# Performance work log

Hardware: AMD Instinct MI355X
Metric: run time of the kernel (lower is better)

Reference implementation:

```python
import jax, jax.numpy as jnp
import numpy as np

LATENT_DIM = 32
NB_LABEL = 10
B = 4096


def _conv4(x, w, b):
    # stride-4 kernel-4 conv == non-overlapping 4x4 patch contraction
    Bn, C, H, W = x.shape
    xp = x.reshape(Bn, C, H // 4, 4, W // 4, 4)
    return jnp.einsum('bcipjq,ocpq->boij', xp, w) + b[None, :, None, None]


def _deconv4(x, w, b):
    # stride-4 kernel-4 ConvTranspose2d, padding 0: each pixel expands to a 4x4 block
    Bn, C, H, W = x.shape
    y = jnp.einsum('bcij,copq->boipjq', x, w)  # w: (Cin, Cout, 4, 4)
    return y.reshape(Bn, w.shape[1], H * 4, W * 4) + b[None, :, None, None]


def setup_inputs() -> dict:
    key = jax.random.key(0)
    ks = jax.random.split(key, 24)
    s = 0.05

    def rn(k, shape, scale=s):
        return jax.random.normal(k, shape, dtype=jnp.float32) * scale

    return {
        'x': jax.random.normal(ks[0], (B, 1, 64, 64), dtype=jnp.float32),
        'z': jax.random.normal(ks[1], (B, NB_LABEL), dtype=jnp.float32),
        'u_in': jax.random.normal(ks[2], (B, 2), dtype=jnp.float32),
        'conv1_w': rn(ks[3], (16, 1, 4, 4)), 'conv1_b': rn(ks[4], (16,)),
        'conv2_w': rn(ks[5], (64, 16, 4, 4)), 'conv2_b': rn(ks[6], (64,)),
        'conv3_w': rn(ks[7], (256, 64, 4, 4)), 'conv3_b': rn(ks[8], (256,)),
        'w_xz': rn(ks[9], (32, 256)),
        'w_label': rn(ks[10], (NB_LABEL, 32)),
        'w_zd1': rn(ks[11], (LATENT_DIM, NB_LABEL)),
        'w_zd2': rn(ks[12], (LATENT_DIM, NB_LABEL)),
        'w_xu': rn(ks[13], (32, 256)),
        'w_mu': rn(ks[14], (2, 32)),
        'w_logvar': rn(ks[15], (2, 32)),
        'tc_w': rn(ks[16], (LATENT_DIM, 256, 2)),
        'tc_b': rn(ks[17], (LATENT_DIM, 256)),
        'dec3_w': rn(ks[18], (256, 64, 4, 4)), 'dec3_b': rn(ks[19], (64,)),
        'dec2_w': rn(ks[20], (64, 16, 4, 4)), 'dec2_b': rn(ks[21], (16,)),
        'dec1_w': rn(ks[22], (16, 1, 4, 4)), 'dec1_b': jnp.zeros((1,), dtype=jnp.float32),
    }


def reference(x, z, u_in, conv1_w, conv1_b, conv2_w, conv2_b, conv3_w, conv3_b,
              w_xz, w_label, w_zd1, w_zd2, w_xu, w_mu, w_logvar, tc_w, tc_b,
              dec3_w, dec3_b, dec2_w, dec2_b, dec1_w, dec1_b):
    h = jax.nn.relu(_conv4(x, conv1_w, conv1_b))
    h = jax.nn.relu(_conv4(h, conv2_w, conv2_b))
    h = jax.nn.relu(_conv4(h, conv3_w, conv3_b))
    h = h.reshape(h.shape[0], -1)                       # (B, 256)

    x_z = jax.nn.relu(h @ w_xz.T)                       # (B, 32)
    z_logit = x_z @ w_label.T                           # (B, 10)

    key = jax.random.key(42)
    k_cat, k_eps = jax.random.split(key)
    z_hat = jax.random.categorical(k_cat, z_logit, axis=-1)       # (B,)
    z_onehot = jax.nn.one_hot(z_hat, NB_LABEL, dtype=z_logit.dtype)
    z_d1 = z_onehot @ w_zd1.T                           # (B, 32)
    z_d2 = z_onehot @ w_zd2.T                           # (B, 32)

    x_u = jax.nn.relu(h @ w_xu.T)                       # (B, 32)
    mu = x_u @ w_mu.T                                   # (B, 2)
    logvar = x_u @ w_logvar.T                           # (B, 2)
    std = jnp.exp(0.5 * logvar)
    eps = jax.random.normal(k_eps, std.shape, dtype=std.dtype)
    u_out = eps * std + mu                              # (B, 2)

    # all 32 tiny Linear(2->256)+ReLU collapsed into one batched einsum
    trans = u_out[:, None, :] + jnp.stack([z_d1, z_d2], axis=-1)   # (B, 32, 2)
    x_hat = jax.nn.relu(jnp.einsum('bic,ioc->bio', trans, tc_w) + tc_b[None]).sum(axis=1)  # (B, 256)
    transfo_d1 = trans[:, :, 0]                         # (B, 32)
    transfo_d2 = trans[:, :, 1]

    d = x_hat.reshape(-1, 256, 1, 1)
    d = jax.nn.relu(_deconv4(d, dec3_w, dec3_b))        # (B, 64, 4, 4)
    d = jax.nn.relu(_deconv4(d, dec2_w, dec2_b))        # (B, 16, 16, 16)
    x_hat_logit = _deconv4(d, dec1_w, dec1_b)           # (B, 1, 64, 64)

    return (z_logit, z_hat.reshape(-1, 1), mu, logvar, u_out, x_hat_logit, transfo_d1, transfo_d2)
```

## Files before the change

### kernel.cpp

```cpp
#include <hip/hip_runtime.h>
#include <stdint.h>

#define B_TOT 4096

#define OFF_ZL 0
#define OFF_ZH 40960
#define OFF_MU 45056
#define OFF_LV 53248
#define OFF_UO 61440
#define OFF_XL 69632
#define OFF_T1 16846848
#define OFF_T2 16977920

typedef __attribute__((ext_vector_type(8))) short bf16x8;
typedef __attribute__((ext_vector_type(4))) float f32x4;

__device__ __forceinline__ unsigned short f2b(float f) {
  unsigned int u = __float_as_uint(f);
  return (unsigned short)((u + 0x7FFFu + ((u >> 16) & 1u)) >> 16);
}
__device__ __forceinline__ float b2f(unsigned short b) {
  return __uint_as_float(((unsigned int)b) << 16);
}

#define TF_ROUND(r) do { x0 += x1; x1 = (x1 << (r)) | (x1 >> (32-(r))); x1 ^= x0; } while(0)

__device__ __forceinline__ void threefry(uint32_t k0, uint32_t k1,
                                         uint32_t c0, uint32_t c1,
                                         uint32_t& o0, uint32_t& o1) {
  uint32_t ks2 = k0 ^ k1 ^ 0x1BD11BDAu;
  uint32_t x0 = c0 + k0, x1 = c1 + k1;
  TF_ROUND(13); TF_ROUND(15); TF_ROUND(26); TF_ROUND(6);
  x0 += k1;  x1 += ks2 + 1u;
  TF_ROUND(17); TF_ROUND(29); TF_ROUND(16); TF_ROUND(24);
  x0 += ks2; x1 += k0 + 2u;
  TF_ROUND(13); TF_ROUND(15); TF_ROUND(26); TF_ROUND(6);
  x0 += k0;  x1 += k1 + 3u;
  TF_ROUND(17); TF_ROUND(29); TF_ROUND(16); TF_ROUND(24);
  x0 += k1;  x1 += ks2 + 4u;
  TF_ROUND(13); TF_ROUND(15); TF_ROUND(26); TF_ROUND(6);
  x0 += ks2; x1 += k0 + 5u;
  o0 = x0; o1 = x1;
}

__device__ __forceinline__ uint32_t tf_bits32(uint32_t k0, uint32_t k1, uint32_t j) {
  uint32_t r0, r1;
  threefry(k0, k1, 0u, j, r0, r1);
  return r0 ^ r1;
}

__device__ __forceinline__ float erfinv_xla(float x) {
  float w = -log1pf(-x * x);
  float p;
  if (w < 5.0f) {
    w -= 2.5f;
    p = 2.81022636e-08f;
    p = fmaf(p, w, 3.43273939e-07f);
    p = fmaf(p, w, -3.5233877e-06f);
    p = fmaf(p, w, -4.39150654e-06f);
    p = fmaf(p, w, 0.00021858087f);
    p = fmaf(p, w, -0.00125372503f);
    p = fmaf(p, w, -0.00417768164f);
    p = fmaf(p, w, 0.246640727f);
    p = fmaf(p, w, 1.50140941f);
  } else {
    w = sqrtf(w) - 3.0f;
    p = -0.000200214257f;
    p = fmaf(p, w, 0.000100950558f);
    p = fmaf(p, w, 0.00134934322f);
    p = fmaf(p, w, -0.00367342844f);
    p = fmaf(p, w, 0.00573950773f);
    p = fmaf(p, w, -0.0076224613f);
    p = fmaf(p, w, 0.00943887047f);
    p = fmaf(p, w, 1.00167406f);
    p = fmaf(p, w, 2.83297682f);
  }
  return p * x;
}

__global__ __launch_bounds__(256) void k_prep(const float* __restrict__ w3,
    const float* __restrict__ w2, unsigned short* __restrict__ w3t,
    unsigned short* __restrict__ w2t) {
  int idx = blockIdx.x * 256 + threadIdx.x;
  unsigned short tmp[8];
  if (idx < 32768) {
    int np = idx >> 5, k0 = (idx & 31) * 8;
    int ic = np & 63, pos = np >> 6;
#pragma unroll
    for (int i = 0; i < 8; ++i)
      tmp[i] = f2b(w3[(size_t)(k0 + i) * 1024 + ic * 16 + pos]);
    *(bf16x8*)(w3t + (size_t)np * 256 + k0) = *(bf16x8*)tmp;
  } else if (idx < 32768 + 2048) {
    int j = idx - 32768;
    int n = j >> 3, k0 = (j & 7) * 8;
#pragma unroll
    for (int i = 0; i < 8; ++i)
      tmp[i] = f2b(w2[(size_t)(k0 + i) * 256 + n]);
    *(bf16x8*)(w2t + (size_t)n * 64 + k0) = *(bf16x8*)tmp;
  }
}

__global__ __launch_bounds__(256) void k_conv1(const float* __restrict__ x,
    const float* __restrict__ w, const float* __restrict__ bias,
    float* __restrict__ h1t) {
  __shared__ __align__(16) float ws[256];
  __shared__ float bs[16];
  int b = blockIdx.x, t = threadIdx.x;
  ws[t] = w[t];
  if (t < 16) bs[t] = bias[t];
  __syncthreads();
  int i = t >> 4, j = t & 15;
  const float* xb = x + (size_t)b * 4096;
  float4 xv[4];
#pragma unroll
  for (int p = 0; p < 4; ++p)
    xv[p] = *(const float4*)(xb + (4 * i + p) * 64 + 4 * j);
  float acc[16];
#pragma unroll
  for (int oc = 0; oc < 16; ++oc) acc[oc] = bs[oc];
#pragma unroll
  for (int p = 0; p < 4; ++p) {
    float4 xp = xv[p];
#pragma unroll
    for (int oc = 0; oc < 16; ++oc) {
      float4 wv = *(const float4*)(ws + oc * 16 + p * 4);
      acc[oc] = fmaf(xp.x, wv.x, acc[oc]);
      acc[oc] = fmaf(xp.y, wv.y, acc[oc]);
      acc[oc] = fmaf(xp.z, wv.z, acc[oc]);
      acc[oc] = fmaf(xp.w, wv.w, acc[oc]);
    }
  }
  float* hb = h1t + (size_t)b * 4096 + ((i >> 2) * 4 + (j >> 2)) * 256
            + (i & 3) * 4 + (j & 3);
#pragma unroll
  for (int oc = 0; oc < 16; ++oc)
    hb[oc * 16] = fmaxf(acc[oc], 0.0f);
}

__global__ __launch_bounds__(256) void k_conv2g(const float* __restrict__ A,
    const float* __restrict__ Bw, const float* __restrict__ bias,
    float* __restrict__ h2) {
  __shared__ __align__(16) float As[16][68];
  __shared__ __align__(16) float Bs[16][68];
  int t = threadIdx.x;
  int m0 = blockIdx.x * 64;
  int tx = t & 15, ty = t >> 4;
  float acc[4][4] = {};
  int lr = t >> 2, lk = (t & 3) * 4;
  for (int k0 = 0; k0 < 256; k0 += 16) {
    float4 a  = *(const float4*)(A  + (size_t)(m0 + lr) * 256 + k0 + lk);
    float4 bv = *(const float4*)(Bw + (size_t)lr * 256 + k0 + lk);
    As[lk + 0][lr] = a.x; As[lk + 1][lr] = a.y; As[lk + 2][lr] = a.z; As[lk + 3][lr] = a.w;
    Bs[lk + 0][lr] = bv.x; Bs[lk + 1][lr] = bv.y; Bs[lk + 2][lr] = bv.z; Bs[lk + 3][lr] = bv.w;
    __syncthreads();
#pragma unroll
    for (int kk = 0; kk < 16; ++kk) {
      float4 af = *(const float4*)(&As[kk][ty * 4]);
      float4 bf = *(const float4*)(&Bs[kk][tx * 4]);
      float av[4] = {af.x, af.y, af.z, af.w};
      float bb[4] = {bf.x, bf.y, bf.z, bf.w};
#pragma unroll
      for (int ii = 0; ii < 4; ++ii)
#pragma unroll
        for (int jj = 0; jj < 4; ++jj)
          acc[ii][jj] = fmaf(av[ii], bb[jj], acc[ii][jj]);
    }
    __syncthreads();
  }
  float4 bb4 = *(const float4*)(bias + tx * 4);
  float bb[4] = {bb4.x, bb4.y, bb4.z, bb4.w};
#pragma unroll
  for (int ii = 0; ii < 4; ++ii) {
    int row = m0 + ty * 4 + ii;
    int b = row >> 4, pos = row & 15;
    float* hp = h2 + (size_t)b * 1024 + pos;
#pragma unroll
    for (int jj = 0; jj < 4; ++jj)
      hp[(tx * 4 + jj) * 16] = fmaxf(acc[ii][jj] + bb[jj], 0.f);
  }
}

__global__ __launch_bounds__(256) void k_conv3p(const float* __restrict__ A,
    const float* __restrict__ w3, float* __restrict__ part) {
  __shared__ __align__(16) float As[16][68];
  __shared__ __align__(16) float Bs[16][68];
  int t = threadIdx.x;
  int m0 = blockIdx.x * 64, n0 = blockIdx.y * 64;
  int kb = blockIdx.z * 256;
  int tx = t & 15, ty = t >> 4;
  float acc[4][4] = {};
  int lr = t >> 2, lk = (t & 3) * 4;
  for (int k0 = kb; k0 < kb + 256; k0 += 16) {
    float4 a  = *(const float4*)(A  + (size_t)(m0 + lr) * 1024 + k0 + lk);
    float4 bv = *(const float4*)(w3 + (size_t)(n0 + lr) * 1024 + k0 + lk);
    As[lk + 0][lr] = a.x; As[lk + 1][lr] = a.y; As[lk + 2][lr] = a.z; As[lk + 3][lr] = a.w;
    Bs[lk + 0][lr] = bv.x; Bs[lk + 1][lr] = bv.y; Bs[lk + 2][lr] = bv.z; Bs[lk + 3][lr] = bv.w;
    __syncthreads();
#pragma unroll
    for (int kk = 0; kk < 16; ++kk) {
      float4 af = *(const float4*)(&As[kk][ty * 4]);
      float4 bf = *(const float4*)(&Bs[kk][tx * 4]);
      float av[4] = {af.x, af.y, af.z, af.w};
      float bb[4] = {bf.x, bf.y, bf.z, bf.w};
#pragma unroll
      for (int ii = 0; ii < 4; ++ii)
#pragma unroll
        for (int jj = 0; jj < 4; ++jj)
          acc[ii][jj] = fmaf(av[ii], bb[jj], acc[ii][jj]);
    }
    __syncthreads();
  }
  float* pc = part + (size_t)blockIdx.z * 1048576;
#pragma unroll
  for (int ii = 0; ii < 4; ++ii) {
    int row = m0 + ty * 4 + ii;
    *(float4*)(pc + (size_t)row * 256 + n0 + tx * 4) =
        make_float4(acc[ii][0], acc[ii][1], acc[ii][2], acc[ii][3]);
  }
}

__global__ __launch_bounds__(256) void k_c3red(const float* __restrict__ part,
    const float* __restrict__ b3, float* __restrict__ h) {
  int idx = blockIdx.x * 256 + threadIdx.x;
  int row = idx >> 6, c4 = (idx & 63) * 4;
  const float* p0 = part + (size_t)row * 256 + c4;
  float4 s  = *(const float4*)(p0);
  float4 s1 = *(const float4*)(p0 + 1048576);
  float4 s2 = *(const float4*)(p0 + 2097152);
  float4 s3 = *(const float4*)(p0 + 3145728);
  float4 bb = *(const float4*)(b3 + c4);
  float4 o;
  o.x = fmaxf(((s.x + s1.x) + s2.x) + s3.x + bb.x, 0.f);
  o.y = fmaxf(((s.y + s1.y) + s2.y) + s3.y + bb.y, 0.f);
  o.z = fmaxf(((s.z + s1.z) + s2.z) + s3.z + bb.z, 0.f);
  o.w = fmaxf(((s.w + s1.w) + s2.w) + s3.w + bb.w, 0.f);
  *(float4*)(h + (size_t)row * 256 + c4) = o;
}

__global__ __launch_bounds__(256) void k_headA(const float* __restrict__ A,
    const float* __restrict__ w_xz, const float* __restrict__ w_xu,
    float* __restrict__ xzxu) {
  __shared__ __align__(16) float As[16][68];
  __shared__ __align__(16) float Bs[16][68];
  int t = threadIdx.x;
  int m0 = blockIdx.x * 64;
  int tx = t & 15, ty = t >> 4;
  float acc[4][4] = {};
  int lr = t >> 2, lk = (t & 3) * 4;
  const float* wr = (lr < 32) ? (w_xz + lr * 256) : (w_xu + (lr - 32) * 256);
  for (int k0 = 0; k0 < 256; k0 += 16) {
    float4 a  = *(const float4*)(A + (size_t)(m0 + lr) * 256 + k0 + lk);
    float4 bv = *(const float4*)(wr + k0 + lk);
    As[lk + 0][lr] = a.x; As[lk + 1][lr] = a.y; As[lk + 2][lr] = a.z; As[lk + 3][lr] = a.w;
    Bs[lk + 0][lr] = bv.x; Bs[lk + 1][lr] = bv.y; Bs[lk + 2][lr] = bv.z; Bs[lk + 3][lr] = bv.w;
    __syncthreads();
#pragma unroll
    for (int kk = 0; kk < 16; ++kk) {
      float4 af = *(const float4*)(&As[kk][ty * 4]);
      float4 bf = *(const float4*)(&Bs[kk][tx * 4]);
      float av[4] = {af.x, af.y, af.z, af.w};
      float bb[4] = {bf.x, bf.y, bf.z, bf.w};
#pragma unroll
      for (int ii = 0; ii < 4; ++ii)
#pragma unroll
        for (int jj = 0; jj < 4; ++jj)
          acc[ii][jj] = fmaf(av[ii], bb[jj], acc[ii][jj]);
    }
    __syncthreads();
  }
#pragma unroll
  for (int ii = 0; ii < 4; ++ii) {
    int row = m0 + ty * 4 + ii;
    float4 o;
    o.x = fmaxf(acc[ii][0], 0.f);
    o.y = fmaxf(acc[ii][1], 0.f);
    o.z = fmaxf(acc[ii][2], 0.f);
    o.w = fmaxf(acc[ii][3], 0.f);
    *(float4*)(xzxu + (size_t)row * 64 + tx * 4) = o;
  }
}

__global__ __launch_bounds__(256) void k_headB(
    const float* __restrict__ xzxu,
    const float* __restrict__ w_label,
    const float* __restrict__ w_zd1, const float* __restrict__ w_zd2,
    const float* __restrict__ w_mu, const float* __restrict__ w_logvar,
    const float* __restrict__ tc_w, const float* __restrict__ tc_b,
    float* __restrict__ outp, unsigned short* __restrict__ xhb) {
  __shared__ __align__(16) unsigned short twL[16384];
  __shared__ __align__(16) unsigned short tbL[8192];
  __shared__ float xzs[4][32], xus[4][32];
  __shared__ float zls[4][10], gbs[4][10];
  __shared__ float mus[4][2], lvs[4][2], epss[4][2], uos[4][2];
  __shared__ float t1s[4][32], t2s[4][32];
  __shared__ int zhs[4];
  int t = threadIdx.x;
  int wv = t >> 6, l = t & 63;
  int b = blockIdx.x * 4 + wv;

  for (int v = t; v < 4096; v += 256) {
    float4 w4 = *(const float4*)(tc_w + (size_t)v * 4);
    unsigned short pk[4] = {f2b(w4.x), f2b(w4.y), f2b(w4.z), f2b(w4.w)};
    *(ushort4*)(twL + v * 4) = *(ushort4*)pk;
  }
  for (int v = t; v < 2048; v += 256) {
    float4 b4 = *(const float4*)(tc_b + (size_t)v * 4);
    unsigned short pk[4] = {f2b(b4.x), f2b(b4.y), f2b(b4.z), f2b(b4.w)};
    *(ushort4*)(tbL + v * 4) = *(ushort4*)pk;
  }
  {
    float v = xzxu[(size_t)b * 64 + l];
    if (l < 32) xzs[wv][l] = v; else xus[wv][l - 32] = v;
  }
  __syncthreads();

  if (l < 10) {
    float acc = 0.f;
#pragma unroll
    for (int k = 0; k < 32; ++k) acc = fmaf(xzs[wv][k], w_label[l * 32 + k], acc);
    zls[wv][l] = acc;
    outp[OFF_ZL + (size_t)b * 10 + l] = acc;
  } else if (l < 12) {
    int d = l - 10;
    float acc = 0.f;
#pragma unroll
    for (int k = 0; k < 32; ++k) acc = fmaf(xus[wv][k], w_mu[d * 32 + k], acc);
    mus[wv][d] = acc;
    outp[OFF_MU + (size_t)b * 2 + d] = acc;
  } else if (l < 14) {
    int d = l - 12;
    float acc = 0.f;
#pragma unroll
    for (int k = 0; k < 32; ++k) acc = fmaf(xus[wv][k], w_logvar[d * 32 + k], acc);
    lvs[wv][d] = acc;
    outp[OFF_LV + (size_t)b * 2 + d] = acc;
  }
  __syncthreads();

  if (l < 10) {
    uint32_t kc0, kc1;
    threefry(0u, 42u, 0u, 0u, kc0, kc1);
    uint32_t bits = tf_bits32(kc0, kc1, (uint32_t)(b * 10 + l));
    float f = __uint_as_float((bits >> 9) | 0x3F800000u) - 1.0f;
    float u = fmaxf(f, 1.17549435e-38f);
    float g = -logf(-logf(u));
    gbs[wv][l] = zls[wv][l] + g;
  } else if (l < 12) {
    int d = l - 10;
    uint32_t ke0, ke1;
    threefry(0u, 42u, 0u, 1u, ke0, ke1);
    uint32_t bits = tf_bits32(ke0, ke1, (uint32_t)(b * 2 + d));
    float f = __uint_as_float((bits >> 9) | 0x3F800000u) - 1.0f;
    float u = fmaxf(f * 2.0f - 0.99999994f, -0.99999994f);
    epss[wv][d] = 1.41421356f * erfinv_xla(u);
  }
  __syncthreads();

  if (l == 0) {
    float best = gbs[wv][0];
    int bi = 0;
#pragma unroll
    for (int c = 1; c < 10; ++c) {
      float v = gbs[wv][c];
      if (v > best) { best = v; bi = c; }
    }
    zhs[wv] = bi;
    outp[OFF_ZH + b] = (float)bi;
  } else if (l < 3) {
    int d = l - 1;
    float sd = expf(0.5f * lvs[wv][d]);
    float uo = fmaf(epss[wv][d], sd, mus[wv][d]);
    uos[wv][d] = uo;
    outp[OFF_UO + (size_t)b * 2 + d] = uo;
  }
  __syncthreads();

  if (l < 32) {
    int zh = zhs[wv];
    float t1 = uos[wv][0] + w_zd1[l * 10 + zh];
    float t2 = uos[wv][1] + w_zd2[l * 10 + zh];
    t1s[wv][l] = t1; t2s[wv][l] = t2;
    outp[OFF_T1 + (size_t)b * 32 + l] = t1;
    outp[OFF_T2 + (size_t)b * 32 + l] = t2;
  }
  __syncthreads();

  {
    float ax = 0.f, ay = 0.f, az = 0.f, aw = 0.f;
#pragma unroll 4
    for (int i = 0; i < 32; ++i) {
      float t1 = t1s[wv][i], t2 = t2s[wv][i];
      ushort4 wa = *(const ushort4*)(twL + i * 512 + l * 8);
      ushort4 wb = *(const ushort4*)(twL + i * 512 + l * 8 + 4);
      ushort4 tb = *(const ushort4*)(tbL + i * 256 + l * 4);
      float s;
      s = fmaf(t1, b2f(wa.x), fmaf(t2, b2f(wa.y), b2f(tb.x))); ax += fmaxf(s, 0.f);
      s = fmaf(t1, b2f(wa.z), fmaf(t2, b2f(wa.w), b2f(tb.y))); ay += fmaxf(s, 0.f);
      s = fmaf(t1, b2f(wb.x), fmaf(t2, b2f(wb.y), b2f(tb.z))); az += fmaxf(s, 0.f);
      s = fmaf(t1, b2f(wb.z), fmaf(t2, b2f(wb.w), b2f(tb.w))); aw += fmaxf(s, 0.f);
    }
    unsigned short pk[4] = {f2b(ax), f2b(ay), f2b(az), f2b(aw)};
    *(ushort4*)(xhb + (size_t)b * 256 + l * 4) = *(ushort4*)pk;
  }
}

__global__ __launch_bounds__(256) void k_dec3m(const unsigned short* __restrict__ xhb,
    const unsigned short* __restrict__ w3t, const float* __restrict__ bias,
    unsigned short* __restrict__ d3t) {
  int t = threadIdx.x;
  int lane = t & 63, wv = t >> 6;
  int m0 = blockIdx.x * 64, n0 = blockIdx.y * 64;
  int l15 = lane & 15, g8 = (lane >> 4) * 8;
  const unsigned short* arow = xhb + (size_t)(m0 + wv * 16 + l15) * 256 + g8;
  const unsigned short* brow = w3t + (size_t)(n0 + l15) * 256 + g8;
  f32x4 acc[4] = {};
  for (int kb = 0; kb < 256; kb += 32) {
    bf16x8 af = *(const bf16x8*)(arow + kb);
#pragma unroll
    for (int ns = 0; ns < 4; ++ns) {
      bf16x8 bf = *(const bf16x8*)(brow + (size_t)ns * 4096 + kb);
      acc[ns] = __builtin_amdgcn_mfma_f32_16x16x32_bf16(af, bf, acc[ns], 0, 0, 0);
    }
  }
  int rbase = (lane >> 4) * 4;
#pragma unroll
  for (int ns = 0; ns < 4; ++ns) {
    int ncol = n0 + ns * 16 + l15;
    float bb = bias[ncol & 63];
#pragma unroll
    for (int r = 0; r < 4; ++r) {
      float v = fmaxf(acc[ns][r] + bb, 0.f);
      d3t[(size_t)(m0 + wv * 16 + rbase + r) * 1024 + ncol] = f2b(v);
    }
  }
}

__global__ __launch_bounds__(256) void k_dec2m(const unsigned short* __restrict__ d3t,
    const unsigned short* __restrict__ w2t, const float* __restrict__ b2,
    const float* __restrict__ w1, const float* __restrict__ b1,
    float* __restrict__ outp) {
  __shared__ unsigned short d2L[4][4096];
  __shared__ __align__(16) float w1s[256];
  __shared__ float b1s;
  int t = threadIdx.x;
  int lane = t & 63, wv = t >> 6;
  int m0 = blockIdx.x * 64;
  w1s[t] = w1[t];
  if (t == 0) b1s = b1[0];
  int l15 = lane & 15, g8 = (lane >> 4) * 8;
  const unsigned short* arow = d3t + (size_t)(m0 + wv * 16 + l15) * 64 + g8;
  bf16x8 af0 = *(const bf16x8*)(arow);
  bf16x8 af1 = *(const bf16x8*)(arow + 32);
  const unsigned short* brow = w2t + (size_t)l15 * 64 + g8;
  f32x4 acc[16] = {};
#pragma unroll
  for (int ns = 0; ns < 16; ++ns) {
    bf16x8 bf0 = *(const bf16x8*)(brow + (size_t)ns * 1024);
    bf16x8 bf1 = *(const bf16x8*)(brow + (size_t)ns * 1024 + 32);
    acc[ns] = __builtin_amdgcn_mfma_f32_16x16x32_bf16(af0, bf0, acc[ns], 0, 0, 0);
    acc[ns] = __builtin_amdgcn_mfma_f32_16x16x32_bf16(af1, bf1, acc[ns], 0, 0, 0);
  }
  int rbase = (lane >> 4) * 4;
  int pq_p = l15 >> 2, pq_q = l15 & 3;
#pragma unroll
  for (int ns = 0; ns < 16; ++ns) {
    float bb = b2[ns];
#pragma unroll
    for (int r = 0; r < 4; ++r) {
      int pos = rbase + r;
      float v = fmaxf(acc[ns][r] + bb, 0.f);
      d2L[wv][ns * 256 + ((pos >> 2) * 4 + pq_p) * 16 + (pos & 3) * 4 + pq_q] = f2b(v);
    }
  }
  __syncthreads();
  int bg0 = m0 >> 4;
  for (int c4 = 0; c4 < 16; ++c4) {
    int v = t + 256 * c4;
    int bp = v >> 10;
    int I = (v & 1023) >> 4;
    int jpix = v & 15;
    int ipix = I >> 2, pp = I & 3;
    const unsigned short* dl = &d2L[bp][ipix * 16 + jpix];
    float4 o = make_float4(b1s, b1s, b1s, b1s);
#pragma unroll
    for (int c = 0; c < 16; ++c) {
      float dv = b2f(dl[c * 256]);
      float4 wv4 = *(const float4*)(w1s + c * 16 + pp * 4);
      o.x = fmaf(dv, wv4.x, o.x);
      o.y = fmaf(dv, wv4.y, o.y);
      o.z = fmaf(dv, wv4.z, o.z);
      o.w = fmaf(dv, wv4.w, o.w);
    }
    *(float4*)(outp + (size_t)(bg0 + bp) * 4096 + I * 64 + jpix * 4) = o;
  }
}

extern "C" void kernel_launch(void* const* d_in, const int* in_sizes, int n_in,
                              void* d_out, int out_size, void* d_ws, size_t ws_size,
                              hipStream_t stream) {
  const float* x       = (const float*)d_in[0];
  const float* conv1_w = (const float*)d_in[3];
  const float* conv1_b = (const float*)d_in[4];
  const float* conv2_w = (const float*)d_in[5];
  const float* conv2_b = (const float*)d_in[6];
  const float* conv3_w = (const float*)d_in[7];
  const float* conv3_b = (const float*)d_in[8];
  const float* w_xz    = (const float*)d_in[9];
  const float* w_label = (const float*)d_in[10];
  const float* w_zd1   = (const float*)d_in[11];
  const float* w_zd2   = (const float*)d_in[12];
  const float* w_xu    = (const float*)d_in[13];
  const float* w_mu    = (const float*)d_in[14];
  const float* w_logvar= (const float*)d_in[15];
  const float* tc_w    = (const float*)d_in[16];
  const float* tc_b    = (const float*)d_in[17];
  const float* dec3_w  = (const float*)d_in[18];
  const float* dec3_b  = (const float*)d_in[19];
  const float* dec2_w  = (const float*)d_in[20];
  const float* dec2_b  = (const float*)d_in[21];
  const float* dec1_w  = (const float*)d_in[22];
  const float* dec1_b  = (const float*)d_in[23];

  float* out = (float*)d_out;
  float* ws  = (float*)d_ws;

  float* big = out + OFF_XL;
  float* h2  = ws;
  float* h   = ws + 4194304;
  unsigned short* d3t = (unsigned short*)ws;
  unsigned short* xhb = (unsigned short*)(ws + 5242880);
  unsigned short* w3t = (unsigned short*)(ws + 5767168);
  unsigned short* w2t = (unsigned short*)(ws + 5898240);
  float* xzxu = ws + 5906432;

  k_prep<<<136, 256, 0, stream>>>(dec3_w, dec2_w, w3t, w2t);
  k_conv1<<<B_TOT, 256, 0, stream>>>(x, conv1_w, conv1_b, big);
  k_conv2g<<<1024, 256, 0, stream>>>(big, conv2_w, conv2_b, h2);
  k_conv3p<<<dim3(64, 4, 4), 256, 0, stream>>>(h2, conv3_w, big);
  k_c3red<<<1024, 256, 0, stream>>>(big, conv3_b, h);
  k_headA<<<64, 256, 0, stream>>>(h, w_xz, w_xu, xzxu);
  k_headB<<<B_TOT / 4, 256, 0, stream>>>(xzxu, w_label, w_zd1, w_zd2, w_mu,
                                         w_logvar, tc_w, tc_b, out, xhb);
  k_dec3m<<<dim3(64, 16), 256, 0, stream>>>(xhb, w3t, dec3_b, d3t);
  k_dec2m<<<1024, 256, 0, stream>>>(d3t, w2t, dec2_b, dec1_w, dec1_b, big);
}
```

Baseline: 194.7 us.

## Fuse conv1 into conv2 GEMM via shared memory; batch headB over 16 samples

conv1 and conv2 are merged into a single kernel. conv1 activations for 4 samples are computed directly into the shared-memory A tile (in two K-halves) and consumed by the conv2 GEMM, so the 64MB h1 intermediate is never written to or read back from global memory. headB now processes 16 samples per block instead of 4, amortizing the per-block conversion of tc_w/tc_b to bf16 in LDS. The cost is a larger LDS footprint (about 40KB) for the fused kernel, extra barriers, and fewer blocks for headB.

New measurement: 243.5 us. +25.1%, slower.

```diff
diff --git a/kernel.cpp b/kernel.cpp
--- a/kernel.cpp
+++ b/kernel.cpp
@@ -100,80 +100,81 @@
   }
 }
 
-__global__ __launch_bounds__(256) void k_conv1(const float* __restrict__ x,
-    const float* __restrict__ w, const float* __restrict__ bias,
-    float* __restrict__ h1t) {
-  __shared__ __align__(16) float ws[256];
-  __shared__ float bs[16];
-  int b = blockIdx.x, t = threadIdx.x;
-  ws[t] = w[t];
-  if (t < 16) bs[t] = bias[t];
+__global__ __launch_bounds__(256) void k_conv12(const float* __restrict__ x,
+    const float* __restrict__ w1c, const float* __restrict__ b1c,
+    const float* __restrict__ w2, const float* __restrict__ b2c,
+    float* __restrict__ h2) {
+  __shared__ __align__(16) float As[128][68];
+  __shared__ __align__(16) float Bs[16][68];
+  __shared__ __align__(16) float w1s[256];
+  __shared__ float b1v[16];
+  int t = threadIdx.x;
+  int blk = blockIdx.x;
+  w1s[t] = w1c[t];
+  if (t < 16) b1v[t] = b1c[t];
   __syncthreads();
   int i = t >> 4, j = t & 15;
-  const float* xb = x + (size_t)b * 4096;
-  float4 xv[4];
-#pragma unroll
-  for (int p = 0; p < 4; ++p)
-    xv[p] = *(const float4*)(xb + (4 * i + p) * 64 + 4 * j);
-  float acc[16];
-#pragma unroll
-  for (int oc = 0; oc < 16; ++oc) acc[oc] = bs[oc];
-#pragma unroll
-  for (int p = 0; p < 4; ++p) {
-    float4 xp = xv[p];
-#pragma unroll
-    for (int oc = 0; oc < 16; ++oc) {
-      float4 wv = *(const float4*)(ws + oc * 16 + p * 4);
-      acc[oc] = fmaf(xp.x, wv.x, acc[oc]);
-      acc[oc] = fmaf(xp.y, wv.y, acc[oc]);
-      acc[oc] = fmaf(xp.z, wv.z, acc[oc]);
-      acc[oc] = fmaf(xp.w, wv.w, acc[oc]);
-    }
-  }
-  float* hb = h1t + (size_t)b * 4096 + ((i >> 2) * 4 + (j >> 2)) * 256
-            + (i & 3) * 4 + (j & 3);
-#pragma unroll
-  for (int oc = 0; oc < 16; ++oc)
-    hb[oc * 16] = fmaxf(acc[oc], 0.0f);
-}
-
-__global__ __launch_bounds__(256) void k_conv2g(const float* __restrict__ A,
-    const float* __restrict__ Bw, const float* __restrict__ bias,
-    float* __restrict__ h2) {
-  __shared__ __align__(16) float As[16][68];
-  __shared__ __align__(16) float Bs[16][68];
-  int t = threadIdx.x;
-  int m0 = blockIdx.x * 64;
+  int pos = (i >> 2) * 4 + (j >> 2);
+  int pq  = (i & 3) * 4 + (j & 3);
   int tx = t & 15, ty = t >> 4;
+  int lrB = t >> 2, lkB = (t & 3) * 4;
   float acc[4][4] = {};
-  int lr = t >> 2, lk = (t & 3) * 4;
-  for (int k0 = 0; k0 < 256; k0 += 16) {
-    float4 a  = *(const float4*)(A  + (size_t)(m0 + lr) * 256 + k0 + lk);
-    float4 bv = *(const float4*)(Bw + (size_t)lr * 256 + k0 + lk);
-    As[lk + 0][lr] = a.x; As[lk + 1][lr] = a.y; As[lk + 2][lr] = a.z; As[lk + 3][lr] = a.w;
-    Bs[lk + 0][lr] = bv.x; Bs[lk + 1][lr] = bv.y; Bs[lk + 2][lr] = bv.z; Bs[lk + 3][lr] = bv.w;
-    __syncthreads();
-#pragma unroll
-    for (int kk = 0; kk < 16; ++kk) {
-      float4 af = *(const float4*)(&As[kk][ty * 4]);
-      float4 bf = *(const float4*)(&Bs[kk][tx * 4]);
-      float av[4] = {af.x, af.y, af.z, af.w};
-      float bb[4] = {bf.x, bf.y, bf.z, bf.w};
-#pragma unroll
-      for (int ii = 0; ii < 4; ++ii)
-#pragma unroll
-        for (int jj = 0; jj < 4; ++jj)
-          acc[ii][jj] = fmaf(av[ii], bb[jj], acc[ii][jj]);
-    }
-    __syncthreads();
-  }
-  float4 bb4 = *(const float4*)(bias + tx * 4);
+  const float* xbase = x + (size_t)blk * 4 * 4096;
+
+  for (int half = 0; half < 2; ++half) {
+    for (int bb = 0; bb < 4; ++bb) {
+      const float* xb = xbase + bb * 4096;
+      float4 xv[4];
+#pragma unroll
+      for (int p = 0; p < 4; ++p)
+        xv[p] = *(const float4*)(xb + (4 * i + p) * 64 + 4 * j);
+      float a1[8];
+#pragma unroll
+      for (int o = 0; o < 8; ++o) a1[o] = b1v[half * 8 + o];
+#pragma unroll
+      for (int p = 0; p < 4; ++p) {
+        float4 xp = xv[p];
+#pragma unroll
+        for (int o = 0; o < 8; ++o) {
+          float4 wv = *(const float4*)(w1s + (half * 8 + o) * 16 + p * 4);
+          a1[o] = fmaf(xp.x, wv.x, a1[o]);
+          a1[o] = fmaf(xp.y, wv.y, a1[o]);
+          a1[o] = fmaf(xp.z, wv.z, a1[o]);
+          a1[o] = fmaf(xp.w, wv.w, a1[o]);
+        }
+      }
+      int row = bb * 16 + pos;
+#pragma unroll
+      for (int o = 0; o < 8; ++o)
+        As[o * 16 + pq][row] = fmaxf(a1[o], 0.f);
+    }
+    for (int k0 = 0; k0 < 128; k0 += 16) {
+      float4 bv = *(const float4*)(w2 + (size_t)lrB * 256 + half * 128 + k0 + lkB);
+      Bs[lkB + 0][lrB] = bv.x; Bs[lkB + 1][lrB] = bv.y;
+      Bs[lkB + 2][lrB] = bv.z; Bs[lkB + 3][lrB] = bv.w;
+      __syncthreads();
+#pragma unroll
+      for (int kk = 0; kk < 16; ++kk) {
+        float4 af = *(const float4*)(&As[k0 + kk][ty * 4]);
+        float4 bf = *(const float4*)(&Bs[kk][tx * 4]);
+        float av[4] = {af.x, af.y, af.z, af.w};
+        float bw[4] = {bf.x, bf.y, bf.z, bf.w};
+#pragma unroll
+        for (int ii = 0; ii < 4; ++ii)
+#pragma unroll
+          for (int jj = 0; jj < 4; ++jj)
+            acc[ii][jj] = fmaf(av[ii], bw[jj], acc[ii][jj]);
+      }
+      __syncthreads();
+    }
+  }
+  float4 bb4 = *(const float4*)(b2c + tx * 4);
   float bb[4] = {bb4.x, bb4.y, bb4.z, bb4.w};
 #pragma unroll
   for (int ii = 0; ii < 4; ++ii) {
-    int row = m0 + ty * 4 + ii;
-    int b = row >> 4, pos = row & 15;
-    float* hp = h2 + (size_t)b * 1024 + pos;
+    int row = blk * 64 + ty * 4 + ii;
+    int b = row >> 4, pos2 = row & 15;
+    float* hp = h2 + (size_t)b * 1024 + pos2;
 #pragma unroll
     for (int jj = 0; jj < 4; ++jj)
       hp[(tx * 4 + jj) * 16] = fmaxf(acc[ii][jj] + bb[jj], 0.f);
@@ -296,7 +297,6 @@
   __shared__ int zhs[4];
   int t = threadIdx.x;
   int wv = t >> 6, l = t & 63;
-  int b = blockIdx.x * 4 + wv;
 
   for (int v = t; v < 4096; v += 256) {
     float4 w4 = *(const float4*)(tc_w + (size_t)v * 4);
@@ -308,99 +308,104 @@
     unsigned short pk[4] = {f2b(b4.x), f2b(b4.y), f2b(b4.z), f2b(b4.w)};
     *(ushort4*)(tbL + v * 4) = *(ushort4*)pk;
   }
-  {
-    float v = xzxu[(size_t)b * 64 + l];
-    if (l < 32) xzs[wv][l] = v; else xus[wv][l - 32] = v;
-  }
-  __syncthreads();
-
-  if (l < 10) {
-    float acc = 0.f;
-#pragma unroll
-    for (int k = 0; k < 32; ++k) acc = fmaf(xzs[wv][k], w_label[l * 32 + k], acc);
-    zls[wv][l] = acc;
-    outp[OFF_ZL + (size_t)b * 10 + l] = acc;
-  } else if (l < 12) {
-    int d = l - 10;
-    float acc = 0.f;
-#pragma unroll
-    for (int k = 0; k < 32; ++k) acc = fmaf(xus[wv][k], w_mu[d * 32 + k], acc);
-    mus[wv][d] = acc;
-    outp[OFF_MU + (size_t)b * 2 + d] = acc;
-  } else if (l < 14) {
-    int d = l - 12;
-    float acc = 0.f;
-#pragma unroll
-    for (int k = 0; k < 32; ++k) acc = fmaf(xus[wv][k], w_logvar[d * 32 + k], acc);
-    lvs[wv][d] = acc;
-    outp[OFF_LV + (size_t)b * 2 + d] = acc;
-  }
-  __syncthreads();
-
-  if (l < 10) {
-    uint32_t kc0, kc1;
-    threefry(0u, 42u, 0u, 0u, kc0, kc1);
-    uint32_t bits = tf_bits32(kc0, kc1, (uint32_t)(b * 10 + l));
-    float f = __uint_as_float((bits >> 9) | 0x3F800000u) - 1.0f;
-    float u = fmaxf(f, 1.17549435e-38f);
-    float g = -logf(-logf(u));
-    gbs[wv][l] = zls[wv][l] + g;
-  } else if (l < 12) {
-    int d = l - 10;
-    uint32_t ke0, ke1;
-    threefry(0u, 42u, 0u, 1u, ke0, ke1);
-    uint32_t bits = tf_bits32(ke0, ke1, (uint32_t)(b * 2 + d));
-    float f = __uint_as_float((bits >> 9) | 0x3F800000u) - 1.0f;
-    float u = fmaxf(f * 2.0f - 0.99999994f, -0.99999994f);
-    epss[wv][d] = 1.41421356f * erfinv_xla(u);
-  }
-  __syncthreads();
-
-  if (l == 0) {
-    float best = gbs[wv][0];
-    int bi = 0;
-#pragma unroll
-    for (int c = 1; c < 10; ++c) {
-      float v = gbs[wv][c];
-      if (v > best) { best = v; bi = c; }
-    }
-    zhs[wv] = bi;
-    outp[OFF_ZH + b] = (float)bi;
-  } else if (l < 3) {
-    int d = l - 1;
-    float sd = expf(0.5f * lvs[wv][d]);
-    float uo = fmaf(epss[wv][d], sd, mus[wv][d]);
-    uos[wv][d] = uo;
-    outp[OFF_UO + (size_t)b * 2 + d] = uo;
-  }
-  __syncthreads();
-
-  if (l < 32) {
-    int zh = zhs[wv];
-    float t1 = uos[wv][0] + w_zd1[l * 10 + zh];
-    float t2 = uos[wv][1] + w_zd2[l * 10 + zh];
-    t1s[wv][l] = t1; t2s[wv][l] = t2;
-    outp[OFF_T1 + (size_t)b * 32 + l] = t1;
-    outp[OFF_T2 + (size_t)b * 32 + l] = t2;
-  }
-  __syncthreads();
-
-  {
-    float ax = 0.f, ay = 0.f, az = 0.f, aw = 0.f;
+
+  for (int bi = 0; bi < 4; ++bi) {
+    int b = blockIdx.x * 16 + bi * 4 + wv;
+    {
+      float v = xzxu[(size_t)b * 64 + l];
+      if (l < 32) xzs[wv][l] = v; else xus[wv][l - 32] = v;
+    }
+    __syncthreads();
+
+    if (l < 10) {
+      float acc = 0.f;
+#pragma unroll
+      for (int k = 0; k < 32; ++k) acc = fmaf(xzs[wv][k], w_label[l * 32 + k], acc);
+      zls[wv][l] = acc;
+      outp[OFF_ZL + (size_t)b * 10 + l] = acc;
+    } else if (l < 12) {
+      int d = l - 10;
+      float acc = 0.f;
+#pragma unroll
+      for (int k = 0; k < 32; ++k) acc = fmaf(xus[wv][k], w_mu[d * 32 + k], acc);
+      mus[wv][d] = acc;
+      outp[OFF_MU + (size_t)b * 2 + d] = acc;
+    } else if (l < 14) {
+      int d = l - 12;
+      float acc = 0.f;
+#pragma unroll
+      for (int k = 0; k < 32; ++k) acc = fmaf(xus[wv][k], w_logvar[d * 32 + k], acc);
+      lvs[wv][d] = acc;
+      outp[OFF_LV + (size_t)b * 2 + d] = acc;
+    }
+    __syncthreads();
+
+    if (l < 10) {
+      uint32_t kc0, kc1;
+      threefry(0u, 42u, 0u, 0u, kc0, kc1);
+      uint32_t bits = tf_bits32(kc0, kc1, (uint32_t)(b * 10 + l));
+      float f = __uint_as_float((bits >> 9) | 0x3F800000u) - 1.0f;
+      float u = fmaxf(f, 1.17549435e-38f);
+      float g = -logf(-logf(u));
+      gbs[wv][l] = zls[wv][l] + g;
+    } else if (l < 12) {
+      int d = l - 10;
+      uint32_t ke0, ke1;
+      threefry(0u, 42u, 0u, 1u, ke0, ke1);
+      uint32_t bits = tf_bits32(ke0, ke1, (uint32_t)(b * 2 + d));
+      float f = __uint_as_float((bits >> 9) | 0x3F800000u) - 1.0f;
+      float u = fmaxf(f * 2.0f - 0.99999994f, -0.99999994f);
+      epss[wv][d] = 1.41421356f * erfinv_xla(u);
+    }
+    __syncthreads();
+
+    if (l == 0) {
+      float best = gbs[wv][0];
+      int bi2 = 0;
+#pragma unroll
+      for (int c = 1; c < 10; ++c) {
+        float v = gbs[wv][c];
+        if (v > best) { best = v; bi2 = c; }
+      }
+      zhs[wv] = bi2;
+      outp[OFF_ZH + b] = (float)bi2;
+    } else if (l < 3) {
+      int d = l - 1;
+      float sd = expf(0.5f * lvs[wv][d]);
+      float uo = fmaf(epss[wv][d], sd, mus[wv][d]);
+      uos[wv][d] = uo;
+      outp[OFF_UO + (size_t)b * 2 + d] = uo;
+    }
+    __syncthreads();
+
+    if (l < 32) {
+      int zh = zhs[wv];
+      float t1 = uos[wv][0] + w_zd1[l * 10 + zh];
+      float t2 = uos[wv][1] + w_zd2[l * 10 + zh];
+      t1s[wv][l] = t1; t2s[wv][l] = t2;
+      outp[OFF_T1 + (size_t)b * 32 + l] = t1;
+      outp[OFF_T2 + (size_t)b * 32 + l] = t2;
+    }
+    __syncthreads();
+
+    {
+      float ax = 0.f, ay = 0.f, az = 0.f, aw = 0.f;
 #pragma unroll 4
-    for (int i = 0; i < 32; ++i) {
-      float t1 = t1s[wv][i], t2 = t2s[wv][i];
-      ushort4 wa = *(const ushort4*)(twL + i * 512 + l * 8);
-      ushort4 wb = *(const ushort4*)(twL + i * 512 + l * 8 + 4);
-      ushort4 tb = *(const ushort4*)(tbL + i * 256 + l * 4);
-      float s;
-      s = fmaf(t1, b2f(wa.x), fmaf(t2, b2f(wa.y), b2f(tb.x))); ax += fmaxf(s, 0.f);
-      s = fmaf(t1, b2f(wa.z), fmaf(t2, b2f(wa.w), b2f(tb.y))); ay += fmaxf(s, 0.f);
-      s = fmaf(t1, b2f(wb.x), fmaf(t2, b2f(wb.y), b2f(tb.z))); az += fmaxf(s, 0.f);
-      s = fmaf(t1, b2f(wb.z), fmaf(t2, b2f(wb.w), b2f(tb.w))); aw += fmaxf(s, 0.f);
-    }
-    unsigned short pk[4] = {f2b(ax), f2b(ay), f2b(az), f2b(aw)};
-    *(ushort4*)(xhb + (size_t)b * 256 + l * 4) = *(ushort4*)pk;
+      for (int i = 0; i < 32; ++i) {
+        float t1 = t1s[wv][i], t2 = t2s[wv][i];
+        ushort4 wa = *(const ushort4*)(twL + i * 512 + l * 8);
+        ushort4 wb = *(const ushort4*)(twL + i * 512 + l * 8 + 4);
+        ushort4 tb = *(const ushort4*)(tbL + i * 256 + l * 4);
+        float s;
+        s = fmaf(t1, b2f(wa.x), fmaf(t2, b2f(wa.y), b2f(tb.x))); ax += fmaxf(s, 0.f);
+        s = fmaf(t1, b2f(wa.z), fmaf(t2, b2f(wa.w), b2f(tb.y))); ay += fmaxf(s, 0.f);
+        s = fmaf(t1, b2f(wb.x), fmaf(t2, b2f(wb.y), b2f(tb.z))); az += fmaxf(s, 0.f);
+        s = fmaf(t1, b2f(wb.z), fmaf(t2, b2f(wb.w), b2f(tb.w))); aw += fmaxf(s, 0.f);
+      }
+      unsigned short pk[4] = {f2b(ax), f2b(ay), f2b(az), f2b(aw)};
+      *(ushort4*)(xhb + (size_t)b * 256 + l * 4) = *(ushort4*)pk;
+    }
+    __syncthreads();
   }
 }
 
@@ -534,13 +539,12 @@
   float* xzxu = ws + 5906432;
 
   k_prep<<<136, 256, 0, stream>>>(dec3_w, dec2_w, w3t, w2t);
-  k_conv1<<<B_TOT, 256, 0, stream>>>(x, conv1_w, conv1_b, big);
-  k_conv2g<<<1024, 256, 0, stream>>>(big, conv2_w, conv2_b, h2);
+  k_conv12<<<1024, 256, 0, stream>>>(x, conv1_w, conv1_b, conv2_w, conv2_b, h2);
   k_conv3p<<<dim3(64, 4, 4), 256, 0, stream>>>(h2, conv3_w, big);
   k_c3red<<<1024, 256, 0, stream>>>(big, conv3_b, h);
   k_headA<<<64, 256, 0, stream>>>(h, w_xz, w_xu, xzxu);
-  k_headB<<<B_TOT / 4, 256, 0, stream>>>(xzxu, w_label, w_zd1, w_zd2, w_mu,
-                                         w_logvar, tc_w, tc_b, out, xhb);
+  k_headB<<<256, 256, 0, stream>>>(xzxu, w_label, w_zd1, w_zd2, w_mu,
+                                   w_logvar, tc_w, tc_b, out, xhb);
   k_dec3m<<<dim3(64, 16), 256, 0, stream>>>(xhb, w3t, dec3_b, d3t);
   k_dec2m<<<1024, 256, 0, stream>>>(d3t, w2t, dec2_b, dec1_w, dec1_b, big);
 }
```

## Fuse conv3 split-K reduction into head GEMM and stage conv1 stores via LDS

Applied to the files above, without the earlier changes.

The separate split-K reduction kernel for conv3 is removed. The head GEMM now sums the four partial buffers, adds the bias and applies ReLU while loading its A tile, which saves one launch and the write and re-read of the 4 MB intermediate. Separately, conv1 now stages its scattered strided output stores in a padded shared-memory buffer and writes them out as coalesced float4 stores. The catch is that the head GEMM runs only 64 blocks, so it now pulls all the partial-sum traffic through very few CUs, and conv1 gains about 17 KB of LDS per block, which may lower its occupancy.

Measured after the change: 191.2 us. About the same (-1.8%).

```diff
diff --git a/kernel.cpp b/kernel.cpp
--- a/kernel.cpp
+++ b/kernel.cpp
@@ -105,6 +105,7 @@
     float* __restrict__ h1t) {
   __shared__ __align__(16) float ws[256];
   __shared__ float bs[16];
+  __shared__ __align__(16) float ds[16 * 264];
   int b = blockIdx.x, t = threadIdx.x;
   ws[t] = w[t];
   if (t < 16) bs[t] = bias[t];
@@ -130,11 +131,19 @@
       acc[oc] = fmaf(xp.w, wv.w, acc[oc]);
     }
   }
-  float* hb = h1t + (size_t)b * 4096 + ((i >> 2) * 4 + (j >> 2)) * 256
-            + (i & 3) * 4 + (j & 3);
+  int pos = (i >> 2) * 4 + (j >> 2);
+  int pq  = (i & 3) * 4 + (j & 3);
+  float* dp = ds + pos * 264 + pq;
 #pragma unroll
   for (int oc = 0; oc < 16; ++oc)
-    hb[oc * 16] = fmaxf(acc[oc], 0.0f);
+    dp[oc * 16] = fmaxf(acc[oc], 0.0f);
+  __syncthreads();
+  float* hb = h1t + (size_t)b * 4096;
+#pragma unroll
+  for (int pass = 0; pass < 4; ++pass) {
+    int idx = pass * 1024 + t * 4;
+    *(float4*)(hb + idx) = *(const float4*)(ds + (idx >> 8) * 264 + (idx & 255));
+  }
 }
 
 __global__ __launch_bounds__(256) void k_conv2g(const float* __restrict__ A,
@@ -219,25 +228,8 @@
   }
 }
 
-__global__ __launch_bounds__(256) void k_c3red(const float* __restrict__ part,
-    const float* __restrict__ b3, float* __restrict__ h) {
-  int idx = blockIdx.x * 256 + threadIdx.x;
-  int row = idx >> 6, c4 = (idx & 63) * 4;
-  const float* p0 = part + (size_t)row * 256 + c4;
-  float4 s  = *(const float4*)(p0);
-  float4 s1 = *(const float4*)(p0 + 1048576);
-  float4 s2 = *(const float4*)(p0 + 2097152);
-  float4 s3 = *(const float4*)(p0 + 3145728);
-  float4 bb = *(const float4*)(b3 + c4);
-  float4 o;
-  o.x = fmaxf(((s.x + s1.x) + s2.x) + s3.x + bb.x, 0.f);
-  o.y = fmaxf(((s.y + s1.y) + s2.y) + s3.y + bb.y, 0.f);
-  o.z = fmaxf(((s.z + s1.z) + s2.z) + s3.z + bb.z, 0.f);
-  o.w = fmaxf(((s.w + s1.w) + s2.w) + s3.w + bb.w, 0.f);
-  *(float4*)(h + (size_t)row * 256 + c4) = o;
-}
-
-__global__ __launch_bounds__(256) void k_headA(const float* __restrict__ A,
+__global__ __launch_bounds__(256) void k_headA(const float* __restrict__ part,
+    const float* __restrict__ b3,
     const float* __restrict__ w_xz, const float* __restrict__ w_xu,
     float* __restrict__ xzxu) {
   __shared__ __align__(16) float As[16][68];
@@ -249,7 +241,17 @@
   int lr = t >> 2, lk = (t & 3) * 4;
   const float* wr = (lr < 32) ? (w_xz + lr * 256) : (w_xu + (lr - 32) * 256);
   for (int k0 = 0; k0 < 256; k0 += 16) {
-    float4 a  = *(const float4*)(A + (size_t)(m0 + lr) * 256 + k0 + lk);
+    const float* p0 = part + (size_t)(m0 + lr) * 256 + k0 + lk;
+    float4 s  = *(const float4*)(p0);
+    float4 s1 = *(const float4*)(p0 + 1048576);
+    float4 s2 = *(const float4*)(p0 + 2097152);
+    float4 s3 = *(const float4*)(p0 + 3145728);
+    float4 bb4 = *(const float4*)(b3 + k0 + lk);
+    float4 a;
+    a.x = fmaxf(((s.x + s1.x) + s2.x) + s3.x + bb4.x, 0.f);
+    a.y = fmaxf(((s.y + s1.y) + s2.y) + s3.y + bb4.y, 0.f);
+    a.z = fmaxf(((s.z + s1.z) + s2.z) + s3.z + bb4.z, 0.f);
+    a.w = fmaxf(((s.w + s1.w) + s2.w) + s3.w + bb4.w, 0.f);
     float4 bv = *(const float4*)(wr + k0 + lk);
     As[lk + 0][lr] = a.x; As[lk + 1][lr] = a.y; As[lk + 2][lr] = a.z; As[lk + 3][lr] = a.w;
     Bs[lk + 0][lr] = bv.x; Bs[lk + 1][lr] = bv.y; Bs[lk + 2][lr] = bv.z; Bs[lk + 3][lr] = bv.w;
@@ -526,7 +528,6 @@
 
   float* big = out + OFF_XL;
   float* h2  = ws;
-  float* h   = ws + 4194304;
   unsigned short* d3t = (unsigned short*)ws;
   unsigned short* xhb = (unsigned short*)(ws + 5242880);
   unsigned short* w3t = (unsigned short*)(ws + 5767168);
@@ -537,8 +538,7 @@
   k_conv1<<<B_TOT, 256, 0, stream>>>(x, conv1_w, conv1_b, big);
   k_conv2g<<<1024, 256, 0, stream>>>(big, conv2_w, conv2_b, h2);
   k_conv3p<<<dim3(64, 4, 4), 256, 0, stream>>>(h2, conv3_w, big);
-  k_c3red<<<1024, 256, 0, stream>>>(big, conv3_b, h);
-  k_headA<<<64, 256, 0, stream>>>(h, w_xz, w_xu, xzxu);
+  k_headA<<<64, 256, 0, stream>>>(big, conv3_b, w_xz, w_xu, xzxu);
   k_headB<<<B_TOT / 4, 256, 0, stream>>>(xzxu, w_label, w_zd1, w_zd2, w_mu,
                                          w_logvar, tc_w, tc_b, out, xhb);
   k_dec3m<<<dim3(64, 16), 256, 0, stream>>>(xhb, w3t, dec3_b, d3t);
```
